# Optimization experiments

Hardware: AMD Instinct MI355X
Metric: run time of the kernel (lower is better)

Reference implementation:

```python
import jax, jax.numpy as jnp
import numpy as np

N_NODES = 50000
N_EDGES = 800000
IN_DIM = 256
HEADS = 4
HID = 64
NEG_SLOPE = 0.2


def setup_inputs() -> dict:
    key = jax.random.key(0)
    ks = jax.random.split(key, 6)
    x = jax.random.normal(ks[0], (N_NODES, IN_DIM), dtype=jnp.float32)
    W = jax.random.normal(ks[1], (IN_DIM, HEADS * HID), dtype=jnp.float32) * 0.05
    attn_l = jax.random.normal(ks[2], (HEADS, HID), dtype=jnp.float32) * 0.05
    attn_r = jax.random.normal(ks[3], (HEADS, HID), dtype=jnp.float32) * 0.05
    src = jax.random.randint(ks[4], (N_EDGES,), 0, N_NODES, dtype=jnp.int32)
    dst = jax.random.randint(ks[5], (N_EDGES,), 0, N_NODES, dtype=jnp.int32)
    return {"x": x, "W": W, "attn_l": attn_l, "attn_r": attn_r, "src": src, "dst": dst}


def reference(x, W, attn_l, attn_r, src, dst):
    N = x.shape[0]
    # Dense projection: [N, H, D]
    feat = (x @ W).reshape(N, HEADS, HID)
    # Per-node attention logits per head: [N, H]
    el = jnp.einsum('nhd,hd->nh', feat, attn_l)
    er = jnp.einsum('nhd,hd->nh', feat, attn_r)
    # Edge scores: gather + leaky_relu, [E, H]
    e = jax.nn.leaky_relu(el[src] + er[dst], negative_slope=NEG_SLOPE)
    # Edge softmax normalized over incoming edges of each destination node
    m = jax.ops.segment_max(e, dst, num_segments=N)           # [N, H]
    m = jnp.where(jnp.isfinite(m), m, jnp.zeros_like(m))      # zero in-degree nodes
    ex = jnp.exp(e - m[dst])                                  # [E, H]
    denom = jax.ops.segment_sum(ex, dst, num_segments=N)      # [N, H]
    alpha = ex / denom[dst]                                   # [E, H]
    # Message + scatter-sum aggregation: [N, H, D]
    msg = feat[src] * alpha[:, :, None]                       # [E, H, D]
    out = jax.ops.segment_sum(msg, dst, num_segments=N)
    # Mean over heads: [N, D]
    return out.mean(axis=1)
```

## Files before the change

kernel.cpp:

```cpp
#include <hip/hip_runtime.h>
#include <hip/hip_bf16.h>

#define IN_DIM 256
#define HEADS 4
#define HID 64
#define NEG_SLOPE 0.2f

typedef float f32x4 __attribute__((ext_vector_type(4)));
typedef short bf16x8 __attribute__((ext_vector_type(8)));
typedef unsigned short u16x8 __attribute__((ext_vector_type(8)));

__device__ __forceinline__ unsigned short f2bf(float f) {
    unsigned u = __float_as_uint(f);
    unsigned r = u + 0x7fffu + ((u >> 16) & 1u);
    return (unsigned short)(r >> 16);
}
__device__ __forceinline__ float bf2f(unsigned short b) {
    return __uint_as_float(((unsigned)b) << 16);
}
__device__ __forceinline__ void gload16(const void* g, void* l) {
    __builtin_amdgcn_global_load_lds(
        (const __attribute__((address_space(1))) unsigned int*)g,
        (__attribute__((address_space(3))) unsigned int*)l, 16, 0, 0);
}

__global__ __launch_bounds__(256) void prep_kernel(
        const float* __restrict__ x, unsigned short* __restrict__ xb, int n8,
        const float* __restrict__ W, unsigned short* __restrict__ wt,
        const int* __restrict__ dst, int* __restrict__ count, int E) {
    const int gsz = gridDim.x * 256;
    const int g0 = blockIdx.x * 256 + threadIdx.x;
    for (int i = g0; i < n8; i += gsz) {
        const float4* p = (const float4*)x + (size_t)i * 2;
        float4 a = p[0], b = p[1];
        u16x8 o;
        o[0] = f2bf(a.x); o[1] = f2bf(a.y); o[2] = f2bf(a.z); o[3] = f2bf(a.w);
        o[4] = f2bf(b.x); o[5] = f2bf(b.y); o[6] = f2bf(b.z); o[7] = f2bf(b.w);
        *(u16x8*)(xb + (size_t)i * 8) = o;
    }
    for (int i = g0; i < 256 * 256; i += gsz) {
        int n = i & 255, k = i >> 8;
        wt[n * 256 + k] = f2bf(W[k * 256 + n]);
    }
    for (int i = g0; i < E; i += gsz) atomicAdd(&count[dst[i]], 1);
}

#define BM 64
#define BK 64
__global__ __launch_bounds__(256) void mfma_gemm_kernel(
        const unsigned short* __restrict__ xb, const unsigned short* __restrict__ wt,
        const float* __restrict__ attn_l, const float* __restrict__ attn_r,
        unsigned short* __restrict__ featb, float* __restrict__ el,
        float* __restrict__ er, int N) {
    __shared__ unsigned short As[BM * BK];
    __shared__ unsigned short Bs[256 * BK];
    const int tid = threadIdx.x;
    const int lane = tid & 63;
    const int wv = tid >> 6;
    const int bm = blockIdx.x * BM;

    f32x4 acc[4][4] = {};

    for (int k0 = 0; k0 < IN_DIM; k0 += BK) {
        #pragma unroll
        for (int r = 0; r < 2; ++r) {
            int i = r * 256 + tid;
            int row = i >> 3, slot = (i & 7) ^ (row & 7);
            int grow = bm + row; if (grow >= N) grow = N - 1;
            gload16(xb + (size_t)grow * IN_DIM + k0 + slot * 8,
                    (char*)As + (size_t)(r * 256 + (wv << 6)) * 16);
        }
        #pragma unroll
        for (int r = 0; r < 8; ++r) {
            int i = r * 256 + tid;
            int row = i >> 3, slot = (i & 7) ^ (row & 7);
            gload16(wt + (size_t)row * IN_DIM + k0 + slot * 8,
                    (char*)Bs + (size_t)(r * 256 + (wv << 6)) * 16);
        }
        __syncthreads();
        #pragma unroll
        for (int kk = 0; kk < 2; ++kk) {
            const int k16 = kk * 4 + (lane >> 4);
            bf16x8 af[4], bg[4];
            #pragma unroll
            for (int m = 0; m < 4; ++m) {
                int row = m * 16 + (lane & 15);
                af[m] = *(const bf16x8*)((const char*)As + row * 128 + ((k16 ^ (row & 7)) << 4));
            }
            #pragma unroll
            for (int n = 0; n < 4; ++n) {
                int row = (wv << 6) + n * 16 + (lane & 15);
                bg[n] = *(const bf16x8*)((const char*)Bs + row * 128 + ((k16 ^ (row & 7)) << 4));
            }
            #pragma unroll
            for (int m = 0; m < 4; ++m)
                #pragma unroll
                for (int n = 0; n < 4; ++n)
                    acc[m][n] = __builtin_amdgcn_mfma_f32_16x16x32_bf16(af[m], bg[n], acc[m][n], 0, 0, 0);
        }
        __syncthreads();
    }

    const int c15 = lane & 15;
    float al0 = attn_l[(wv << 6) + c15],      ar0 = attn_r[(wv << 6) + c15];
    float al1 = attn_l[(wv << 6) + 16 + c15], ar1 = attn_r[(wv << 6) + 16 + c15];
    float al2 = attn_l[(wv << 6) + 32 + c15], ar2 = attn_r[(wv << 6) + 32 + c15];
    float al3 = attn_l[(wv << 6) + 48 + c15], ar3 = attn_r[(wv << 6) + 48 + c15];

    #pragma unroll
    for (int m = 0; m < 4; ++m) {
        #pragma unroll
        for (int j = 0; j < 4; ++j) {
            int row = bm + m * 16 + ((lane >> 4) << 2) + j;
            bool ok = row < N;
            if (ok) {
                #pragma unroll
                for (int n = 0; n < 4; ++n)
                    featb[(size_t)row * IN_DIM + (wv << 6) + n * 16 + c15] = f2bf(acc[m][n][j]);
            }
            float pl = acc[m][0][j] * al0 + acc[m][1][j] * al1 + acc[m][2][j] * al2 + acc[m][3][j] * al3;
            float pr = acc[m][0][j] * ar0 + acc[m][1][j] * ar1 + acc[m][2][j] * ar2 + acc[m][3][j] * ar3;
            #pragma unroll
            for (int off = 1; off < 16; off <<= 1) {
                pl += __shfl_xor(pl, off);
                pr += __shfl_xor(pr, off);
            }
            if (ok && c15 == 0) {
                el[row * HEADS + wv] = pl;
                er[row * HEADS + wv] = pr;
            }
        }
    }
}

__global__ __launch_bounds__(256) void scanA_kernel(
        const int* __restrict__ count, int* __restrict__ bsum, int N) {
    __shared__ int ws[4];
    int tid = threadIdx.x, lane = tid & 63, wv = tid >> 6;
    int i = blockIdx.x * 256 + tid;
    int v = (i < N) ? count[i] : 0;
    #pragma unroll
    for (int off = 1; off < 64; off <<= 1) v += __shfl_xor(v, off);
    if (lane == 0) ws[wv] = v;
    __syncthreads();
    if (tid == 0) bsum[blockIdx.x] = ws[0] + ws[1] + ws[2] + ws[3];
}

__global__ __launch_bounds__(256) void scanC_kernel(
        const int* __restrict__ count, const int* __restrict__ bsum,
        int* __restrict__ row_start, int* __restrict__ cursor, int N) {
    __shared__ int ws[4];
    __shared__ int boff_s;
    int tid = threadIdx.x, lane = tid & 63, wv = tid >> 6;
    int bv = (tid < (int)blockIdx.x) ? bsum[tid] : 0;
    #pragma unroll
    for (int off = 1; off < 64; off <<= 1) bv += __shfl_xor(bv, off);
    if (lane == 0) ws[wv] = bv;
    __syncthreads();
    if (tid == 0) boff_s = ws[0] + ws[1] + ws[2] + ws[3];
    __syncthreads();
    int i = blockIdx.x * 256 + tid;
    int v = (i < N) ? count[i] : 0;
    int incl = v;
    #pragma unroll
    for (int off = 1; off < 64; off <<= 1) {
        int t = __shfl_up(incl, off);
        if (lane >= off) incl += t;
    }
    if (lane == 63) ws[wv] = incl;
    __syncthreads();
    int wofs = 0;
    #pragma unroll
    for (int w = 0; w < 4; ++w) if (w < wv) wofs += ws[w];
    int excl = boff_s + wofs + incl - v;
    if (i < N) { row_start[i] = excl; cursor[i] = excl; }
    else if (i == N) row_start[N] = excl;
}

__global__ __launch_bounds__(256) void scatter_kernel(
        const int* __restrict__ src, const int* __restrict__ dst,
        int* __restrict__ cursor, int* __restrict__ perm_src, int E) {
    int i = blockIdx.x * blockDim.x + threadIdx.x;
    if (i < E) {
        int pos = atomicAdd(&cursor[dst[i]], 1);
        perm_src[pos] = src[i];
    }
}

#define AGG_ONE(s) do {                                             \
    float v_ = el[(s) * HEADS + h] + erh;                           \
    v_ = v_ > 0.f ? v_ : NEG_SLOPE * v_;                            \
    float e_ = __expf(v_);                                          \
    dh += e_;                                                       \
    ushort4 fv_ = *(const ushort4*)(featb + ((size_t)(s) << 8) + col); \
    ax += e_ * bf2f(fv_.x); ay += e_ * bf2f(fv_.y);                 \
    az += e_ * bf2f(fv_.z); aw += e_ * bf2f(fv_.w); } while (0)

__global__ __launch_bounds__(256) void node_aggregate_kernel(
        const unsigned short* __restrict__ featb, const float* __restrict__ el,
        const float* __restrict__ er, const int* __restrict__ row_start,
        const int* __restrict__ perm_src, float* __restrict__ out, int N) {
    int wid = blockIdx.x * 4 + (threadIdx.x >> 6);
    int lane = threadIdx.x & 63;
    if (wid >= N) return;
    const int beg = row_start[wid], end = row_start[wid + 1];
    if (beg == end) {
        if (lane < 16) *(float4*)(out + (size_t)wid * HID + lane * 4) = make_float4(0.f, 0.f, 0.f, 0.f);
        return;
    }
    const int h = lane >> 4;
    const float erh = er[wid * HEADS + h];
    const int col = lane * 4;

    float dh = 0.f, ax = 0.f, ay = 0.f, az = 0.f, aw = 0.f;
    int p = beg;
    while (p < end && (p & 3)) { AGG_ONE(perm_src[p]); ++p; }
    for (; p + 8 <= end; p += 8) {
        int4 pa = *(const int4*)(perm_src + p);
        int4 pb = *(const int4*)(perm_src + p + 4);
        int s0 = pa.x, s1 = pa.y, s2 = pa.z, s3 = pa.w;
        int s4 = pb.x, s5 = pb.y, s6 = pb.z, s7 = pb.w;
        float l0 = el[s0 * HEADS + h], l1 = el[s1 * HEADS + h];
        float l2 = el[s2 * HEADS + h], l3 = el[s3 * HEADS + h];
        float l4 = el[s4 * HEADS + h], l5 = el[s5 * HEADS + h];
        float l6 = el[s6 * HEADS + h], l7 = el[s7 * HEADS + h];
        ushort4 f0 = *(const ushort4*)(featb + ((size_t)s0 << 8) + col);
        ushort4 f1 = *(const ushort4*)(featb + ((size_t)s1 << 8) + col);
        ushort4 f2 = *(const ushort4*)(featb + ((size_t)s2 << 8) + col);
        ushort4 f3 = *(const ushort4*)(featb + ((size_t)s3 << 8) + col);
        ushort4 f4 = *(const ushort4*)(featb + ((size_t)s4 << 8) + col);
        ushort4 f5 = *(const ushort4*)(featb + ((size_t)s5 << 8) + col);
        ushort4 f6 = *(const ushort4*)(featb + ((size_t)s6 << 8) + col);
        ushort4 f7 = *(const ushort4*)(featb + ((size_t)s7 << 8) + col);
        float v0 = l0 + erh, v1 = l1 + erh, v2 = l2 + erh, v3 = l3 + erh;
        float v4 = l4 + erh, v5 = l5 + erh, v6 = l6 + erh, v7 = l7 + erh;
        v0 = v0 > 0.f ? v0 : NEG_SLOPE * v0;  v1 = v1 > 0.f ? v1 : NEG_SLOPE * v1;
        v2 = v2 > 0.f ? v2 : NEG_SLOPE * v2;  v3 = v3 > 0.f ? v3 : NEG_SLOPE * v3;
        v4 = v4 > 0.f ? v4 : NEG_SLOPE * v4;  v5 = v5 > 0.f ? v5 : NEG_SLOPE * v5;
        v6 = v6 > 0.f ? v6 : NEG_SLOPE * v6;  v7 = v7 > 0.f ? v7 : NEG_SLOPE * v7;
        float e0 = __expf(v0), e1 = __expf(v1), e2 = __expf(v2), e3 = __expf(v3);
        float e4 = __expf(v4), e5 = __expf(v5), e6 = __expf(v6), e7 = __expf(v7);
        dh += ((e0 + e1) + (e2 + e3)) + ((e4 + e5) + (e6 + e7));
        ax += e0 * bf2f(f0.x) + e1 * bf2f(f1.x) + e2 * bf2f(f2.x) + e3 * bf2f(f3.x)
            + e4 * bf2f(f4.x) + e5 * bf2f(f5.x) + e6 * bf2f(f6.x) + e7 * bf2f(f7.x);
        ay += e0 * bf2f(f0.y) + e1 * bf2f(f1.y) + e2 * bf2f(f2.y) + e3 * bf2f(f3.y)
            + e4 * bf2f(f4.y) + e5 * bf2f(f5.y) + e6 * bf2f(f6.y) + e7 * bf2f(f7.y);
        az += e0 * bf2f(f0.z) + e1 * bf2f(f1.z) + e2 * bf2f(f2.z) + e3 * bf2f(f3.z)
            + e4 * bf2f(f4.z) + e5 * bf2f(f5.z) + e6 * bf2f(f6.z) + e7 * bf2f(f7.z);
        aw += e0 * bf2f(f0.w) + e1 * bf2f(f1.w) + e2 * bf2f(f2.w) + e3 * bf2f(f3.w)
            + e4 * bf2f(f4.w) + e5 * bf2f(f5.w) + e6 * bf2f(f6.w) + e7 * bf2f(f7.w);
    }
    for (; p + 4 <= end; p += 4) {
        int4 pa = *(const int4*)(perm_src + p);
        AGG_ONE(pa.x); AGG_ONE(pa.y); AGG_ONE(pa.z); AGG_ONE(pa.w);
    }
    while (p < end) { AGG_ONE(perm_src[p]); ++p; }

    float inv = 1.f / dh;
    float rx = ax * inv, ry = ay * inv, rz = az * inv, rw = aw * inv;
    rx += __shfl_xor(rx, 16); ry += __shfl_xor(ry, 16);
    rz += __shfl_xor(rz, 16); rw += __shfl_xor(rw, 16);
    rx += __shfl_xor(rx, 32); ry += __shfl_xor(ry, 32);
    rz += __shfl_xor(rz, 32); rw += __shfl_xor(rw, 32);
    if (lane < 16) {
        *(float4*)(out + (size_t)wid * HID + lane * 4) =
            make_float4(0.25f * rx, 0.25f * ry, 0.25f * rz, 0.25f * rw);
    }
}

extern "C" void kernel_launch(void* const* d_in, const int* in_sizes, int n_in,
                              void* d_out, int out_size, void* d_ws, size_t ws_size,
                              hipStream_t stream) {
    const float* x      = (const float*)d_in[0];
    const float* W      = (const float*)d_in[1];
    const float* attn_l = (const float*)d_in[2];
    const float* attn_r = (const float*)d_in[3];
    const int*   src    = (const int*)d_in[4];
    const int*   dst    = (const int*)d_in[5];
    float* out = (float*)d_out;

    const int N = in_sizes[0] / IN_DIM;
    const int E = in_sizes[4];

    unsigned short* xb    = (unsigned short*)d_ws;
    unsigned short* wtp   = xb + (size_t)N * IN_DIM;
    unsigned short* featb = wtp + 256 * 256;
    float* el        = (float*)(featb + (size_t)N * IN_DIM);
    float* er        = el + (size_t)N * HEADS;
    int*   count     = (int*)(er + (size_t)N * HEADS);
    int*   row_start = count + N;
    int*   cursor    = row_start + N + 4;
    int*   bsum      = cursor + N;
    int*   perm_src  = bsum + 512;

    const int NB = (N + 1 + 255) / 256;

    hipMemsetAsync(count, 0, (size_t)N * sizeof(int), stream);

    prep_kernel<<<2048, 256, 0, stream>>>(x, xb, N * IN_DIM / 8, W, wtp, dst, count, E);

    mfma_gemm_kernel<<<(N + BM - 1) / BM, 256, 0, stream>>>(
        xb, wtp, attn_l, attn_r, featb, el, er, N);

    scanA_kernel<<<NB, 256, 0, stream>>>(count, bsum, N);
    scanC_kernel<<<NB, 256, 0, stream>>>(count, bsum, row_start, cursor, N);
    scatter_kernel<<<(E + 255) / 256, 256, 0, stream>>>(src, dst, cursor, perm_src, E);

    node_aggregate_kernel<<<(N * 64 + 255) / 256, 256, 0, stream>>>(
        featb, el, er, row_start, perm_src, out, N);
}
```

Before: 269.0 us.

## Fuse prep, scan and scatter into one cooperative kernel with grid syncs

```diff
diff --git a/kernel.cpp b/kernel.cpp
--- a/kernel.cpp
+++ b/kernel.cpp
@@ -1,5 +1,8 @@
 #include <hip/hip_runtime.h>
+#include <hip/hip_cooperative_groups.h>
 #include <hip/hip_bf16.h>
+
+namespace cg = cooperative_groups;
 
 #define IN_DIM 256
 #define HEADS 4
@@ -24,12 +27,23 @@
         (__attribute__((address_space(3))) unsigned int*)l, 16, 0, 0);
 }
 
-__global__ __launch_bounds__(256) void prep_kernel(
+__global__ __launch_bounds__(256) void plumbing_kernel(
         const float* __restrict__ x, unsigned short* __restrict__ xb, int n8,
         const float* __restrict__ W, unsigned short* __restrict__ wt,
-        const int* __restrict__ dst, int* __restrict__ count, int E) {
+        const int* __restrict__ src, const int* __restrict__ dst,
+        int* __restrict__ count, int* __restrict__ bsum,
+        int* __restrict__ row_start, int* __restrict__ cursor,
+        int* __restrict__ perm_src, int N, int E, int NB) {
+    cg::grid_group grid = cg::this_grid();
     const int gsz = gridDim.x * 256;
     const int g0 = blockIdx.x * 256 + threadIdx.x;
+    const int tid = threadIdx.x, lane = tid & 63, wv = tid >> 6;
+    __shared__ int ws[4];
+    __shared__ int boff_s;
+
+    for (int i = g0; i < N; i += gsz) count[i] = 0;
+    grid.sync();
+
     for (int i = g0; i < n8; i += gsz) {
         const float4* p = (const float4*)x + (size_t)i * 2;
         float4 a = p[0], b = p[1];
@@ -43,6 +57,52 @@
         wt[n * 256 + k] = f2bf(W[k * 256 + n]);
     }
     for (int i = g0; i < E; i += gsz) atomicAdd(&count[dst[i]], 1);
+    grid.sync();
+
+    for (int c = blockIdx.x; c < NB; c += gridDim.x) {
+        int i = c * 256 + tid;
+        int v = (i < N) ? count[i] : 0;
+        #pragma unroll
+        for (int off = 1; off < 64; off <<= 1) v += __shfl_xor(v, off);
+        if (lane == 0) ws[wv] = v;
+        __syncthreads();
+        if (tid == 0) bsum[c] = ws[0] + ws[1] + ws[2] + ws[3];
+        __syncthreads();
+    }
+    grid.sync();
+
+    for (int c = blockIdx.x; c < NB; c += gridDim.x) {
+        int bv = (tid < c) ? bsum[tid] : 0;
+        #pragma unroll
+        for (int off = 1; off < 64; off <<= 1) bv += __shfl_xor(bv, off);
+        if (lane == 0) ws[wv] = bv;
+        __syncthreads();
+        if (tid == 0) boff_s = ws[0] + ws[1] + ws[2] + ws[3];
+        __syncthreads();
+        int i = c * 256 + tid;
+        int v = (i < N) ? count[i] : 0;
+        int incl = v;
+        #pragma unroll
+        for (int off = 1; off < 64; off <<= 1) {
+            int t = __shfl_up(incl, off);
+            if (lane >= off) incl += t;
+        }
+        if (lane == 63) ws[wv] = incl;
+        __syncthreads();
+        int wofs = 0;
+        #pragma unroll
+        for (int w = 0; w < 4; ++w) if (w < wv) wofs += ws[w];
+        int excl = boff_s + wofs + incl - v;
+        if (i < N) { row_start[i] = excl; cursor[i] = excl; }
+        else if (i == N) row_start[N] = excl;
+        __syncthreads();
+    }
+    grid.sync();
+
+    for (int i = g0; i < E; i += gsz) {
+        int pos = atomicAdd(&cursor[dst[i]], 1);
+        perm_src[pos] = src[i];
+    }
 }
 
 #define BM 64
@@ -133,60 +193,6 @@
     }
 }
 
-__global__ __launch_bounds__(256) void scanA_kernel(
-        const int* __restrict__ count, int* __restrict__ bsum, int N) {
-    __shared__ int ws[4];
-    int tid = threadIdx.x, lane = tid & 63, wv = tid >> 6;
-    int i = blockIdx.x * 256 + tid;
-    int v = (i < N) ? count[i] : 0;
-    #pragma unroll
-    for (int off = 1; off < 64; off <<= 1) v += __shfl_xor(v, off);
-    if (lane == 0) ws[wv] = v;
-    __syncthreads();
-    if (tid == 0) bsum[blockIdx.x] = ws[0] + ws[1] + ws[2] + ws[3];
-}
-
-__global__ __launch_bounds__(256) void scanC_kernel(
-        const int* __restrict__ count, const int* __restrict__ bsum,
-        int* __restrict__ row_start, int* __restrict__ cursor, int N) {
-    __shared__ int ws[4];
-    __shared__ int boff_s;
-    int tid = threadIdx.x, lane = tid & 63, wv = tid >> 6;
-    int bv = (tid < (int)blockIdx.x) ? bsum[tid] : 0;
-    #pragma unroll
-    for (int off = 1; off < 64; off <<= 1) bv += __shfl_xor(bv, off);
-    if (lane == 0) ws[wv] = bv;
-    __syncthreads();
-    if (tid == 0) boff_s = ws[0] + ws[1] + ws[2] + ws[3];
-    __syncthreads();
-    int i = blockIdx.x * 256 + tid;
-    int v = (i < N) ? count[i] : 0;
-    int incl = v;
-    #pragma unroll
-    for (int off = 1; off < 64; off <<= 1) {
-        int t = __shfl_up(incl, off);
-        if (lane >= off) incl += t;
-    }
-    if (lane == 63) ws[wv] = incl;
-    __syncthreads();
-    int wofs = 0;
-    #pragma unroll
-    for (int w = 0; w < 4; ++w) if (w < wv) wofs += ws[w];
-    int excl = boff_s + wofs + incl - v;
-    if (i < N) { row_start[i] = excl; cursor[i] = excl; }
-    else if (i == N) row_start[N] = excl;
-}
-
-__global__ __launch_bounds__(256) void scatter_kernel(
-        const int* __restrict__ src, const int* __restrict__ dst,
-        int* __restrict__ cursor, int* __restrict__ perm_src, int E) {
-    int i = blockIdx.x * blockDim.x + threadIdx.x;
-    if (i < E) {
-        int pos = atomicAdd(&cursor[dst[i]], 1);
-        perm_src[pos] = src[i];
-    }
-}
-
 #define AGG_ONE(s) do {                                             \
     float v_ = el[(s) * HEADS + h] + erh;                           \
     v_ = v_ > 0.f ? v_ : NEG_SLOPE * v_;                            \
@@ -215,44 +221,27 @@
     float dh = 0.f, ax = 0.f, ay = 0.f, az = 0.f, aw = 0.f;
     int p = beg;
     while (p < end && (p & 3)) { AGG_ONE(perm_src[p]); ++p; }
-    for (; p + 8 <= end; p += 8) {
+    for (; p + 4 <= end; p += 4) {
         int4 pa = *(const int4*)(perm_src + p);
-        int4 pb = *(const int4*)(perm_src + p + 4);
         int s0 = pa.x, s1 = pa.y, s2 = pa.z, s3 = pa.w;
-        int s4 = pb.x, s5 = pb.y, s6 = pb.z, s7 = pb.w;
         float l0 = el[s0 * HEADS + h], l1 = el[s1 * HEADS + h];
         float l2 = el[s2 * HEADS + h], l3 = el[s3 * HEADS + h];
-        float l4 = el[s4 * HEADS + h], l5 = el[s5 * HEADS + h];
-        float l6 = el[s6 * HEADS + h], l7 = el[s7 * HEADS + h];
         ushort4 f0 = *(const ushort4*)(featb + ((size_t)s0 << 8) + col);
         ushort4 f1 = *(const ushort4*)(featb + ((size_t)s1 << 8) + col);
         ushort4 f2 = *(const ushort4*)(featb + ((size_t)s2 << 8) + col);
         ushort4 f3 = *(const ushort4*)(featb + ((size_t)s3 << 8) + col);
-        ushort4 f4 = *(const ushort4*)(featb + ((size_t)s4 << 8) + col);
-        ushort4 f5 = *(const ushort4*)(featb + ((size_t)s5 << 8) + col);
-        ushort4 f6 = *(const ushort4*)(featb + ((size_t)s6 << 8) + col);
-        ushort4 f7 = *(const ushort4*)(featb + ((size_t)s7 << 8) + col);
         float v0 = l0 + erh, v1 = l1 + erh, v2 = l2 + erh, v3 = l3 + erh;
-        float v4 = l4 + erh, v5 = l5 + erh, v6 = l6 + erh, v7 = l7 + erh;
-        v0 = v0 > 0.f ? v0 : NEG_SLOPE * v0;  v1 = v1 > 0.f ? v1 : NEG_SLOPE * v1;
-        v2 = v2 > 0.f ? v2 : NEG_SLOPE * v2;  v3 = v3 > 0.f ? v3 : NEG_SLOPE * v3;
-        v4 = v4 > 0.f ? v4 : NEG_SLOPE * v4;  v5 = v5 > 0.f ? v5 : NEG_SLOPE * v5;
-        v6 = v6 > 0.f ? v6 : NEG_SLOPE * v6;  v7 = v7 > 0.f ? v7 : NEG_SLOPE * v7;
-        float e0 = __expf(v0), e1 = __expf(v1), e2 = __expf(v2), e3 = __expf(v3);
-        float e4 = __expf(v4), e5 = __expf(v5), e6 = __expf(v6), e7 = __expf(v7);
-        dh += ((e0 + e1) + (e2 + e3)) + ((e4 + e5) + (e6 + e7));
-        ax += e0 * bf2f(f0.x) + e1 * bf2f(f1.x) + e2 * bf2f(f2.x) + e3 * bf2f(f3.x)
-            + e4 * bf2f(f4.x) + e5 * bf2f(f5.x) + e6 * bf2f(f6.x) + e7 * bf2f(f7.x);
-        ay += e0 * bf2f(f0.y) + e1 * bf2f(f1.y) + e2 * bf2f(f2.y) + e3 * bf2f(f3.y)
-            + e4 * bf2f(f4.y) + e5 * bf2f(f5.y) + e6 * bf2f(f6.y) + e7 * bf2f(f7.y);
-        az += e0 * bf2f(f0.z) + e1 * bf2f(f1.z) + e2 * bf2f(f2.z) + e3 * bf2f(f3.z)
-            + e4 * bf2f(f4.z) + e5 * bf2f(f5.z) + e6 * bf2f(f6.z) + e7 * bf2f(f7.z);
-        aw += e0 * bf2f(f0.w) + e1 * bf2f(f1.w) + e2 * bf2f(f2.w) + e3 * bf2f(f3.w)
-            + e4 * bf2f(f4.w) + e5 * bf2f(f5.w) + e6 * bf2f(f6.w) + e7 * bf2f(f7.w);
-    }
-    for (; p + 4 <= end; p += 4) {
-        int4 pa = *(const int4*)(perm_src + p);
-        AGG_ONE(pa.x); AGG_ONE(pa.y); AGG_ONE(pa.z); AGG_ONE(pa.w);
+        v0 = v0 > 0.f ? v0 : NEG_SLOPE * v0;
+        v1 = v1 > 0.f ? v1 : NEG_SLOPE * v1;
+        v2 = v2 > 0.f ? v2 : NEG_SLOPE * v2;
+        v3 = v3 > 0.f ? v3 : NEG_SLOPE * v3;
+        float e0 = __expf(v0), e1 = __expf(v1);
+        float e2 = __expf(v2), e3 = __expf(v3);
+        dh += (e0 + e1) + (e2 + e3);
+        ax += e0 * bf2f(f0.x) + e1 * bf2f(f1.x) + e2 * bf2f(f2.x) + e3 * bf2f(f3.x);
+        ay += e0 * bf2f(f0.y) + e1 * bf2f(f1.y) + e2 * bf2f(f2.y) + e3 * bf2f(f3.y);
+        az += e0 * bf2f(f0.z) + e1 * bf2f(f1.z) + e2 * bf2f(f2.z) + e3 * bf2f(f3.z);
+        aw += e0 * bf2f(f0.w) + e1 * bf2f(f1.w) + e2 * bf2f(f2.w) + e3 * bf2f(f3.w);
     }
     while (p < end) { AGG_ONE(perm_src[p]); ++p; }
 
@@ -279,8 +268,8 @@
     const int*   dst    = (const int*)d_in[5];
     float* out = (float*)d_out;
 
-    const int N = in_sizes[0] / IN_DIM;
-    const int E = in_sizes[4];
+    int N = in_sizes[0] / IN_DIM;
+    int E = in_sizes[4];
 
     unsigned short* xb    = (unsigned short*)d_ws;
     unsigned short* wtp   = xb + (size_t)N * IN_DIM;
@@ -293,19 +282,29 @@
     int*   bsum      = cursor + N;
     int*   perm_src  = bsum + 512;
 
-    const int NB = (N + 1 + 255) / 256;
-
-    hipMemsetAsync(count, 0, (size_t)N * sizeof(int), stream);
-
-    prep_kernel<<<2048, 256, 0, stream>>>(x, xb, N * IN_DIM / 8, W, wtp, dst, count, E);
+    int NB = (N + 1 + 255) / 256;
+    int n8 = N * IN_DIM / 8;
+
+    int maxB = 0;
+    int pgrid = 1024;
+    if (hipOccupancyMaxActiveBlocksPerMultiprocessor(&maxB, plumbing_kernel, 256, 0)
+            == hipSuccess && maxB > 0) {
+        int cap = maxB * 256;
+        if (cap < pgrid) pgrid = cap;
+    }
+    if (pgrid < 256) pgrid = 256;
+    {
+        void* args[] = { (void*)&x, (void*)&xb, (void*)&n8, (void*)&W, (void*)&wtp,
+                         (void*)&src, (void*)&dst, (void*)&count, (void*)&bsum,
+                         (void*)&row_start, (void*)&cursor, (void*)&perm_src,
+                         (void*)&N, (void*)&E, (void*)&NB };
+        hipLaunchCooperativeKernel((void*)plumbing_kernel, dim3(pgrid), dim3(256),
+                                   args, 0, stream);
+    }
 
     mfma_gemm_kernel<<<(N + BM - 1) / BM, 256, 0, stream>>>(
         xb, wtp, attn_l, attn_r, featb, el, er, N);
 
-    scanA_kernel<<<NB, 256, 0, stream>>>(count, bsum, N);
-    scanC_kernel<<<NB, 256, 0, stream>>>(count, bsum, row_start, cursor, N);
-    scatter_kernel<<<(E + 255) / 256, 256, 0, stream>>>(src, dst, cursor, perm_src, E);
-
     node_aggregate_kernel<<<(N * 64 + 255) / 256, 256, 0, stream>>>(
         featb, el, er, row_start, perm_src, out, N);
 }
```

Result: slower. 648.4 us (+141.0%).
